# Kernel optimization log

Hardware: AMD Instinct MI355X
Metric: run time of the kernel (lower is better)

## Reference

```python
import jax, jax.numpy as jnp
import numpy as np

ROPE_BASE = 10000.0


def _rope_cos_sin(n, d, dtype):
    # standard llama-style rotary embedding over head dim d
    inv_freq = 1.0 / (ROPE_BASE ** (jnp.arange(0, d, 2, dtype=jnp.float32) / d))
    t = jnp.arange(n, dtype=jnp.float32)
    freqs = jnp.einsum('n,f->nf', t, inv_freq)          # [N, d/2]
    emb = jnp.concatenate([freqs, freqs], axis=-1)      # [N, d]
    return jnp.cos(emb).astype(dtype), jnp.sin(emb).astype(dtype)


def _rotate_half(x):
    x1, x2 = jnp.split(x, 2, axis=-1)
    return jnp.concatenate([-x2, x1], axis=-1)


def _apply_rope(x, cos, sin):
    # x: [B, H, N, D]; cos/sin: [N, D] broadcast over B, H
    return x * cos + _rotate_half(x) * sin


def setup_inputs() -> dict:
    key = jax.random.key(0)
    k1, k2, k3 = jax.random.split(key, 3)
    B, N, dim = 2, 2048, 1024
    heads, dim_head = 16, 64
    inner = heads * dim_head
    x = jax.random.normal(k1, (B, N, dim), dtype=jnp.float32)
    w_qkv = jax.random.normal(k2, (dim, 3 * inner), dtype=jnp.float32) * (dim ** -0.5)
    w_out = jax.random.normal(k3, (inner, dim), dtype=jnp.float32) * (inner ** -0.5)
    return {"x": x, "w_qkv": w_qkv, "w_out": w_out}


def reference(x, w_qkv, w_out):
    B, N, _ = x.shape
    heads, dim_head = 16, 64
    qkv = jnp.einsum('bnd,de->bne', x, w_qkv)
    q, k, v = jnp.split(qkv, 3, axis=-1)
    def to_heads(t):
        return t.reshape(B, N, heads, dim_head).transpose(0, 2, 1, 3)  # [B,H,N,D]
    q, k, v = to_heads(q), to_heads(k), to_heads(v)
    cos, sin = _rope_cos_sin(N, dim_head, x.dtype)
    q = _apply_rope(q, cos, sin)
    k = _apply_rope(k, cos, sin)
    scale = dim_head ** -0.5
    scores = jnp.einsum('bhqd,bhkd->bhqk', q, k) * scale   # [B,H,N,N], non-causal
    attn = jax.nn.softmax(scores, axis=-1)
    out = jnp.einsum('bhqk,bhkd->bhqd', attn, v)
    out = out.transpose(0, 2, 1, 3).reshape(B, N, heads * dim_head)
    return jnp.einsum('bne,ed->bnd', out, w_out)
```

## Files before the change

kernel.cpp:

```cpp
#include <hip/hip_runtime.h>

typedef __attribute__((ext_vector_type(8))) short bf16x8;
typedef __attribute__((ext_vector_type(4))) float f32x4;

#define MFMA(a, b, c) __builtin_amdgcn_mfma_f32_16x16x32_bf16(a, b, c, 0, 0, 0)

__device__ __forceinline__ unsigned short f2bf(float f) {
    unsigned u = __builtin_bit_cast(unsigned, f);
    u += 0x7fffu + ((u >> 16) & 1u);
    return (unsigned short)(u >> 16);
}

__device__ __forceinline__ void gload16(const unsigned short* g, unsigned short* l) {
    __builtin_amdgcn_global_load_lds(
        (const __attribute__((address_space(1))) void*)g,
        (__attribute__((address_space(3))) void*)l, 16, 0, 0);
}

__device__ __forceinline__ unsigned pack_bf16(float lo, float hi) {
    unsigned a = __builtin_bit_cast(unsigned, lo) + 0x8000u;
    unsigned b = __builtin_bit_cast(unsigned, hi) + 0x8000u;
    return __builtin_amdgcn_perm(b, a, 0x07060302);
}


__global__ __launch_bounds__(256) void cvt_bf16(const float* __restrict__ in,
                                                unsigned short* __restrict__ out, int n) {
    int i = (blockIdx.x * 256 + threadIdx.x) * 4;
    if (i < n) {
        float4 f = *(const float4*)(in + i);
        ushort4 u;
        u.x = f2bf(f.x); u.y = f2bf(f.y); u.z = f2bf(f.z); u.w = f2bf(f.w);
        *(ushort4*)(out + i) = u;
    }
}

__global__ __launch_bounds__(256) void transpose_cvt(const float* __restrict__ in,
                                                     unsigned short* __restrict__ out,
                                                     int R, int C) {
    __shared__ float tile[32][33];
    const int c0 = blockIdx.x * 32, r0 = blockIdx.y * 32;
    const int tr = threadIdx.x >> 3;
    const int j4 = (threadIdx.x & 7) * 4;
    float4 f = *(const float4*)(in + (size_t)(r0 + tr) * C + c0 + j4);
    tile[tr][j4 + 0] = f.x; tile[tr][j4 + 1] = f.y;
    tile[tr][j4 + 2] = f.z; tile[tr][j4 + 3] = f.w;
    __syncthreads();
    ushort4 u;
    u.x = f2bf(tile[j4 + 0][tr]); u.y = f2bf(tile[j4 + 1][tr]);
    u.z = f2bf(tile[j4 + 2][tr]); u.w = f2bf(tile[j4 + 3][tr]);
    *(ushort4*)(out + (size_t)(c0 + tr) * R + r0 + j4) = u;
}

__global__ __launch_bounds__(256) void rope_tab(float* __restrict__ cosT,
                                                float* __restrict__ sinT) {
    int i = blockIdx.x * 256 + threadIdx.x;
    int n = i >> 5, f = i & 31;
    float ang = (float)n * exp2f((float)f * -0.4152410118609203f);
    float s, c;
    sincosf(ang, &s, &c);
    cosT[i] = c; sinT[i] = s;
}


template <int EPI>
__global__ __launch_bounds__(256, 3) void gemm_bt(const unsigned short* __restrict__ A,
                                                  const unsigned short* __restrict__ Bt,
                                                  int K, int Ncols,
                                                  unsigned short* __restrict__ oq,
                                                  unsigned short* __restrict__ ok,
                                                  unsigned short* __restrict__ ovt,
                                                  float* __restrict__ of,
                                                  const float* __restrict__ cosT,
                                                  const float* __restrict__ sinT) {
    __shared__ unsigned short As[2][128 * 32];
    __shared__ unsigned short Bs[2][128 * 32];
    const int tid = threadIdx.x;
    const int w = tid >> 6, lane = tid & 63, quad = lane >> 4, cc = lane & 15;
    const int wm = w >> 1, wn = w & 1;
    const int m0 = blockIdx.y * 128, n0 = blockIdx.x * 128;

    size_t aoff[2], boff[2];
#pragma unroll
    for (int t = 0; t < 2; t++) {
        int S = w * 128 + t * 64 + lane;
        int row = S >> 2;
        int c = (S & 3) ^ ((row >> 1) & 3);
        aoff[t] = (size_t)(m0 + row) * K + c * 8;
        boff[t] = (size_t)(n0 + row) * K + c * 8;
    }

#pragma unroll
    for (int t = 0; t < 2; t++) {
        gload16(A + aoff[t], &As[0][(w * 2 + t) * 512]);
        gload16(Bt + boff[t], &Bs[0][(w * 2 + t) * 512]);
    }
    __syncthreads();

    f32x4 acc[4][4] = {};
    const int rpos = (quad ^ ((cc >> 1) & 3)) * 8;
    const int nkt = K >> 5;

    for (int kt = 0; kt < nkt; kt++) {
        const int pb = kt & 1;
        if (kt < nkt - 1) {
            const int ko = (kt + 1) * 32;
#pragma unroll
            for (int t = 0; t < 2; t++) {
                gload16(A + aoff[t] + ko, &As[pb ^ 1][(w * 2 + t) * 512]);
                gload16(Bt + boff[t] + ko, &Bs[pb ^ 1][(w * 2 + t) * 512]);
            }
        }
        bf16x8 af[4], bf[4];
#pragma unroll
        for (int i = 0; i < 4; i++)
            af[i] = *(const bf16x8*)&As[pb][(wm * 64 + i * 16 + cc) * 32 + rpos];
#pragma unroll
        for (int i = 0; i < 4; i++)
            bf[i] = *(const bf16x8*)&Bs[pb][(wn * 64 + i * 16 + cc) * 32 + rpos];
#pragma unroll
        for (int i = 0; i < 4; i++)
#pragma unroll
            for (int j = 0; j < 4; j++)
                acc[i][j] = MFMA(af[i], bf[j], acc[i][j]);
        __syncthreads();
    }

    if (EPI == 0) {
        const int e0 = n0 + wn * 64;
        const int which = e0 >> 10;
        const int h = (e0 >> 6) & 15;
        if (which < 2) {
            unsigned short* dst = (which == 0) ? oq : ok;
            const float postscale = (which == 0) ? 0.125f : 1.0f;
#pragma unroll
            for (int mf = 0; mf < 4; mf++) {
#pragma unroll
                for (int r = 0; r < 4; r++) {
                    int mg = m0 + wm * 64 + mf * 16 + quad * 4 + r;
                    int nseq = mg & 2047, b = mg >> 11;
                    float vals[4];
#pragma unroll
                    for (int nf = 0; nf < 4; nf++) vals[nf] = acc[mf][nf][r];
                    size_t rowbase = ((size_t)(b * 16 + h) * 2048 + nseq) * 64;
#pragma unroll
                    for (int nf = 0; nf < 4; nf++) {
                        int d = nf * 16 + cc;
                        int f = d & 31;
                        float cs = cosT[nseq * 32 + f];
                        float sn = sinT[nseq * 32 + f];
                        float partner = vals[nf ^ 2];
                        float outv = (vals[nf] * cs +
                                      ((nf < 2) ? -partner : partner) * sn) * postscale;
                        dst[rowbase + d] = f2bf(outv);
                    }
                }
            }
        } else {
#pragma unroll
            for (int mf = 0; mf < 4; mf++) {
                int mg0 = m0 + wm * 64 + mf * 16 + quad * 4;
                int b = mg0 >> 11, nseq = mg0 & 2047;
#pragma unroll
                for (int nf = 0; nf < 4; nf++) {
                    int d = nf * 16 + cc;
                    ushort4 pk;
                    pk.x = f2bf(acc[mf][nf][0]);
                    pk.y = f2bf(acc[mf][nf][1]);
                    pk.z = f2bf(acc[mf][nf][2]);
                    pk.w = f2bf(acc[mf][nf][3]);
                    *(ushort4*)(ovt + ((size_t)(b * 16 + h) * 64 + d) * 2048 + nseq) = pk;
                }
            }
        }
    } else {
#pragma unroll
        for (int mf = 0; mf < 4; mf++)
#pragma unroll
            for (int nf = 0; nf < 4; nf++)
#pragma unroll
                for (int r = 0; r < 4; r++) {
                    int mg = m0 + wm * 64 + mf * 16 + quad * 4 + r;
                    of[(size_t)mg * Ncols + n0 + wn * 64 + nf * 16 + cc] = acc[mf][nf][r];
                }
    }
}


__global__ __launch_bounds__(512, 4) void attn(const unsigned short* __restrict__ q,
                                               const unsigned short* __restrict__ k,
                                               const unsigned short* __restrict__ vt,
                                               unsigned short* __restrict__ o) {
    __shared__ unsigned short ks[2][64 * 64];
    __shared__ unsigned short vs[2][64 * 64];
    __shared__ unsigned short ps[128 * 72];
    __shared__ float rsb[128];
    const int tid = threadIdx.x;
    const int w = tid >> 6, lane = tid & 63, quad = lane >> 4, cc = lane & 15;
    const int bh = blockIdx.x & 31, qt = blockIdx.x >> 5;

    const unsigned short* qg = q + ((size_t)bh * 2048 + qt * 128 + w * 16) * 64;
    bf16x8 aq[2];
#pragma unroll
    for (int kc = 0; kc < 2; kc++)
        aq[kc] = *(const bf16x8*)(qg + cc * 64 + kc * 32 + quad * 8);

    const int S = w * 64 + lane;
    const int row = S >> 3;
    const int c = (S & 7) ^ (row & 7);
    const int koff = row * 64 + c * 8;
    const int voff = row * 2048 + c * 8;

    const unsigned short* kg0 = k + (size_t)bh * 2048 * 64;
    const unsigned short* vg0 = vt + (size_t)bh * 64 * 2048;

    gload16(kg0 + koff, &ks[0][w * 512]);
    gload16(vg0 + voff, &vs[0][w * 512]);
    __syncthreads();

    f32x4 oacc[4] = {};
    float rs = 0.f;

    for (int kt = 0; kt < 32; kt++) {
        const int pb = kt & 1;
        if (kt < 31) {
            const unsigned short* kb = kg0 + (kt + 1) * 4096;
            const unsigned short* vb = vg0 + (kt + 1) * 64;
            gload16(kb + koff, &ks[pb ^ 1][w * 512]);
            gload16(vb + voff, &vs[pb ^ 1][w * 512]);
        }

        f32x4 s2[4] = {};
        __builtin_amdgcn_s_setprio(1);
#pragma unroll
        for (int kc = 0; kc < 2; kc++) {
#pragma unroll
            for (int nf = 0; nf < 4; nf++) {
                bf16x8 bk = *(const bf16x8*)&ks[pb][(nf * 16 + cc) * 64 +
                                                    ((kc * 4 + quad) ^ (cc & 7)) * 8];
                s2[nf] = MFMA(bk, aq[kc], s2[nf]);
            }
        }
        __builtin_amdgcn_s_setprio(0);

#pragma unroll
        for (int nf = 0; nf < 4; nf++) {
            float p0 = __builtin_amdgcn_exp2f(
                __builtin_fmaf(s2[nf][0], 1.44269504f, -11.54156036f));
            float p1 = __builtin_amdgcn_exp2f(
                __builtin_fmaf(s2[nf][1], 1.44269504f, -11.54156036f));
            float p2 = __builtin_amdgcn_exp2f(
                __builtin_fmaf(s2[nf][2], 1.44269504f, -11.54156036f));
            float p3 = __builtin_amdgcn_exp2f(
                __builtin_fmaf(s2[nf][3], 1.44269504f, -11.54156036f));
            rs += (p0 + p1) + (p2 + p3);
            uint2 pk;
            pk.x = pack_bf16(p0, p1);
            pk.y = pack_bf16(p2, p3);
            *(uint2*)&ps[(w * 16 + cc) * 72 + nf * 16 + quad * 4] = pk;
        }

#pragma unroll
        for (int kc = 0; kc < 2; kc++) {
            bf16x8 ap = *(const bf16x8*)&ps[(w * 16 + cc) * 72 + kc * 32 + quad * 8];
            __builtin_amdgcn_s_setprio(1);
#pragma unroll
            for (int df = 0; df < 4; df++) {
                bf16x8 bv = *(const bf16x8*)&vs[pb][(df * 16 + cc) * 64 +
                                                    ((kc * 4 + quad) ^ (cc & 7)) * 8];
                oacc[df] = MFMA(ap, bv, oacc[df]);
            }
            __builtin_amdgcn_s_setprio(0);
        }

        __syncthreads();
    }

    rs += __shfl_xor(rs, 16, 64);
    rs += __shfl_xor(rs, 32, 64);
    if (quad == 0) rsb[w * 16 + cc] = rs;

    {
        f32x4 rv = *(const f32x4*)&rsb[w * 16 + quad * 4];
        f32x4 inv;
#pragma unroll
        for (int r = 0; r < 4; r++) inv[r] = 1.0f / rv[r];
#pragma unroll
        for (int r = 0; r < 4; r++)
#pragma unroll
            for (int df = 0; df < 4; df++)
                ps[(w * 16 + quad * 4 + r) * 72 + df * 16 + cc] =
                    f2bf(oacc[df][r] * inv[r]);
    }
    __syncthreads();
    {
        const int b = bh >> 4, h = bh & 15;
        int row2 = tid >> 2, seg = tid & 3;
        unsigned short* og =
            o + ((size_t)(b * 2048 + qt * 128 + row2)) * 1024 + h * 64 + seg * 16;
#pragma unroll
        for (int j = 0; j < 2; j++)
            *(uint4*)(og + j * 8) = *(const uint4*)&ps[row2 * 72 + seg * 16 + j * 8];
    }
}


extern "C" void kernel_launch(void* const* d_in, const int* in_sizes, int n_in,
                              void* d_out, int out_size, void* d_ws, size_t ws_size,
                              hipStream_t stream) {
    const float* x = (const float*)d_in[0];
    const float* w_qkv = (const float*)d_in[1];
    const float* w_out = (const float*)d_in[2];
    float* out = (float*)d_out;

    unsigned short* xb    = (unsigned short*)d_ws;
    unsigned short* wqkvT = xb + 4096 * 1024;
    unsigned short* woutT = wqkvT + 3072 * 1024;
    unsigned short* qb    = woutT + 1024 * 1024;
    unsigned short* kb    = qb + 2 * 16 * 2048 * 64;
    unsigned short* vtb   = kb + 2 * 16 * 2048 * 64;
    unsigned short* ob    = vtb + 2 * 16 * 2048 * 64;
    float* cosT = (float*)(ob + 4096 * 1024);
    float* sinT = cosT + 2048 * 32;

    rope_tab<<<256, 256, 0, stream>>>(cosT, sinT);
    cvt_bf16<<<4096, 256, 0, stream>>>(x, xb, 4096 * 1024);
    transpose_cvt<<<dim3(96, 32), 256, 0, stream>>>(w_qkv, wqkvT, 1024, 3072);
    transpose_cvt<<<dim3(32, 32), 256, 0, stream>>>(w_out, woutT, 1024, 1024);
    gemm_bt<0><<<dim3(24, 32), 256, 0, stream>>>(xb, wqkvT, 1024, 3072,
                                                 qb, kb, vtb, nullptr, cosT, sinT);
    attn<<<512, 512, 0, stream>>>(qb, kb, vtb, ob);
    gemm_bt<1><<<dim3(8, 32), 256, 0, stream>>>(ob, woutT, 1024, 1024,
                                                nullptr, nullptr, nullptr, out,
                                                nullptr, nullptr);
}
```

Measured before the change: 186.0 us.

## Software-pipeline QK and PV across iterations, keep P in registers via permlane

Restructures the attention loop so that the QK^T MFMAs for tile kt run alongside the PV MFMAs for tile kt-1. V loads are staggered one stage behind K. The softmax probabilities are no longer written to and reread from LDS; they are rearranged into the MFMA A-operand layout in registers with v_permlane32/16_swap. This aims to hide the exp latency and drop the LDS round trip, at the cost of higher register pressure and a correctness dependence on the permlane lane mapping.

```diff
diff --git a/kernel.cpp b/kernel.cpp
--- a/kernel.cpp
+++ b/kernel.cpp
@@ -215,34 +215,34 @@
     const unsigned short* vg0 = vt + (size_t)bh * 64 * 2048;
 
     gload16(kg0 + koff, &ks[0][w * 512]);
-    gload16(vg0 + voff, &vs[0][w * 512]);
     __syncthreads();
 
     f32x4 oacc[4] = {};
     float rs = 0.f;
-
-    for (int kt = 0; kt < 32; kt++) {
-        const int pb = kt & 1;
-        if (kt < 31) {
-            const unsigned short* kb = kg0 + (kt + 1) * 4096;
-            const unsigned short* vb = vg0 + (kt + 1) * 64;
-            gload16(kb + koff, &ks[pb ^ 1][w * 512]);
-            gload16(vb + voff, &vs[pb ^ 1][w * 512]);
-        }
-
-        f32x4 s2[4] = {};
-        __builtin_amdgcn_s_setprio(1);
-#pragma unroll
-        for (int kc = 0; kc < 2; kc++) {
+    bf16x8 apP[2];
+
+    auto qk = [&](const unsigned short* kbuf, f32x4 s2[4]) {
+#pragma unroll
+        for (int kc = 0; kc < 2; kc++)
 #pragma unroll
             for (int nf = 0; nf < 4; nf++) {
-                bf16x8 bk = *(const bf16x8*)&ks[pb][(nf * 16 + cc) * 64 +
-                                                    ((kc * 4 + quad) ^ (cc & 7)) * 8];
+                bf16x8 bk = *(const bf16x8*)&kbuf[(nf * 16 + cc) * 64 +
+                                                  ((kc * 4 + quad) ^ (cc & 7)) * 8];
                 s2[nf] = MFMA(bk, aq[kc], s2[nf]);
             }
-        }
-        __builtin_amdgcn_s_setprio(0);
-
+    };
+    auto pv = [&](const unsigned short* vbuf, const bf16x8 ap[2]) {
+#pragma unroll
+        for (int kc = 0; kc < 2; kc++)
+#pragma unroll
+            for (int df = 0; df < 4; df++) {
+                bf16x8 bv = *(const bf16x8*)&vbuf[(df * 16 + cc) * 64 +
+                                                  ((kc * 4 + quad) ^ (cc & 7)) * 8];
+                oacc[df] = MFMA(ap[kc], bv, oacc[df]);
+            }
+    };
+    auto softmax_pack = [&](const f32x4 s2[4], bf16x8 apC[2]) {
+        unsigned X[4][2];
 #pragma unroll
         for (int nf = 0; nf < 4; nf++) {
             float p0 = __builtin_amdgcn_exp2f(
@@ -254,27 +254,55 @@
             float p3 = __builtin_amdgcn_exp2f(
                 __builtin_fmaf(s2[nf][3], 1.44269504f, -11.54156036f));
             rs += (p0 + p1) + (p2 + p3);
-            uint2 pk;
-            pk.x = pack_bf16(p0, p1);
-            pk.y = pack_bf16(p2, p3);
-            *(uint2*)&ps[(w * 16 + cc) * 72 + nf * 16 + quad * 4] = pk;
+            X[nf][0] = pack_bf16(p0, p1);
+            X[nf][1] = pack_bf16(p2, p3);
         }
-
 #pragma unroll
         for (int kc = 0; kc < 2; kc++) {
-            bf16x8 ap = *(const bf16x8*)&ps[(w * 16 + cc) * 72 + kc * 32 + quad * 8];
-            __builtin_amdgcn_s_setprio(1);
-#pragma unroll
-            for (int df = 0; df < 4; df++) {
-                bf16x8 bv = *(const bf16x8*)&vs[pb][(df * 16 + cc) * 64 +
-                                                    ((kc * 4 + quad) ^ (cc & 7)) * 8];
-                oacc[df] = MFMA(ap, bv, oacc[df]);
-            }
-            __builtin_amdgcn_s_setprio(0);
+            unsigned a0 = X[kc * 2][0], b0 = X[kc * 2 + 1][0];
+            unsigned a1 = X[kc * 2][1], b1 = X[kc * 2 + 1][1];
+            asm("v_permlane32_swap_b32 %0, %1" : "+v"(a0), "+v"(b0));
+            asm("v_permlane16_swap_b32 %0, %1" : "+v"(a0), "+v"(b0));
+            asm("v_permlane32_swap_b32 %0, %1" : "+v"(a1), "+v"(b1));
+            asm("v_permlane16_swap_b32 %0, %1" : "+v"(a1), "+v"(b1));
+            uint4 dd;
+            dd.x = a0; dd.y = a1; dd.z = b0; dd.w = b1;
+            apC[kc] = __builtin_bit_cast(bf16x8, dd);
         }
-
+    };
+
+    gload16(kg0 + 4096 + koff, &ks[1][w * 512]);
+    gload16(vg0 + voff, &vs[0][w * 512]);
+    {
+        f32x4 s2[4] = {};
+        __builtin_amdgcn_s_setprio(1);
+        qk(ks[0], s2);
+        __builtin_amdgcn_s_setprio(0);
+        softmax_pack(s2, apP);
+    }
+    __syncthreads();
+
+    for (int kt = 1; kt < 32; kt++) {
+        if (kt < 31)
+            gload16(kg0 + (kt + 1) * 4096 + koff, &ks[(kt + 1) & 1][w * 512]);
+        gload16(vg0 + kt * 64 + voff, &vs[kt & 1][w * 512]);
+
+        f32x4 s2[4] = {};
+        __builtin_amdgcn_s_setprio(1);
+        qk(ks[kt & 1], s2);
+        pv(vs[(kt - 1) & 1], apP);
+        __builtin_amdgcn_s_setprio(0);
+
+        bf16x8 apC[2];
+        softmax_pack(s2, apC);
+        apP[0] = apC[0];
+        apP[1] = apC[1];
         __syncthreads();
     }
+
+    __builtin_amdgcn_s_setprio(1);
+    pv(vs[1], apP);
+    __builtin_amdgcn_s_setprio(0);
 
     rs += __shfl_xor(rs, 16, 64);
     rs += __shfl_xor(rs, 32, 64);
```

Result: no change. 188.1 us (+1.1%).

## Add dedicated 256x256 QKV GEMM with four-phase LDS pipeline and setprio

Applied to the files above, without the earlier changes.

Replaces the templated 128x128 QKV projection GEMM with a specialised 512-thread kernel. It uses 256x256 tiles, a 64-wide K step, an XOR-swizzled LDS layout and double buffering. Compute is split into four barrier-separated MFMA phases with raised wave priority. The aim is more operand reuse per LDS load and better overlap of global-to-LDS loads with MFMA. The trade-off is only 192 blocks, fewer than the CU count, plus higher register pressure. The output projection is split into its own non-templated kernel.

```diff
diff --git a/kernel.cpp b/kernel.cpp
--- a/kernel.cpp
+++ b/kernel.cpp
@@ -63,16 +63,151 @@
 }
 
 
-template <int EPI>
-__global__ __launch_bounds__(256, 3) void gemm_bt(const unsigned short* __restrict__ A,
-                                                  const unsigned short* __restrict__ Bt,
-                                                  int K, int Ncols,
-                                                  unsigned short* __restrict__ oq,
-                                                  unsigned short* __restrict__ ok,
-                                                  unsigned short* __restrict__ ovt,
-                                                  float* __restrict__ of,
-                                                  const float* __restrict__ cosT,
-                                                  const float* __restrict__ sinT) {
+#define PHASE(AB, BB, MH, NH, DOA, DOB)                                           \
+    do {                                                                          \
+        if (DOA) {                                                                \
+            _Pragma("unroll") for (int mf = 0; mf < 4; mf++)                      \
+                _Pragma("unroll") for (int kc = 0; kc < 2; kc++)                  \
+                    af[mf][kc] = *(const bf16x8*)&(AB)[                           \
+                        (wm * 128 + MH * 64 + mf * 16 + cc) * 64 +                \
+                        ((kc * 4 + quad) ^ (cc & 7)) * 8];                        \
+        }                                                                         \
+        if (DOB) {                                                                \
+            _Pragma("unroll") for (int nf = 0; nf < 2; nf++)                      \
+                _Pragma("unroll") for (int kc = 0; kc < 2; kc++)                  \
+                    bfr[nf][kc] = *(const bf16x8*)&(BB)[                          \
+                        (wn * 64 + NH * 32 + nf * 16 + cc) * 64 +                 \
+                        ((kc * 4 + quad) ^ (cc & 7)) * 8];                        \
+        }                                                                         \
+        __builtin_amdgcn_s_setprio(1);                                            \
+        _Pragma("unroll") for (int mf = 0; mf < 4; mf++)                          \
+            _Pragma("unroll") for (int nf = 0; nf < 2; nf++)                      \
+                _Pragma("unroll") for (int kc = 0; kc < 2; kc++)                  \
+                    acc[MH * 4 + mf][NH * 2 + nf] = MFMA(                         \
+                        af[mf][kc], bfr[nf][kc], acc[MH * 4 + mf][NH * 2 + nf]);  \
+        __builtin_amdgcn_s_setprio(0);                                            \
+    } while (0)
+
+__global__ __launch_bounds__(512, 2) void gemm_qkv(const unsigned short* __restrict__ A,
+                                                   const unsigned short* __restrict__ Bt,
+                                                   unsigned short* __restrict__ oq,
+                                                   unsigned short* __restrict__ ok,
+                                                   unsigned short* __restrict__ ovt,
+                                                   const float* __restrict__ cosT,
+                                                   const float* __restrict__ sinT) {
+    __shared__ unsigned short Ab[2][256 * 64];
+    __shared__ unsigned short Bb[2][256 * 64];
+    const int tid = threadIdx.x;
+    const int w = tid >> 6, lane = tid & 63, quad = lane >> 4, cc = lane & 15;
+    const int wm = w >> 2, wn = w & 3;
+    const int m0 = blockIdx.y * 256, n0 = blockIdx.x * 256;
+
+    int soff[4], lb[4];
+#pragma unroll
+    for (int j = 0; j < 4; j++) {
+        int S = j * 512 + w * 64 + lane;
+        int row = S >> 3;
+        int c = (S & 7) ^ (row & 7);
+        soff[j] = row * 1024 + c * 8;
+        lb[j] = (j * 512 + w * 64) * 8;
+    }
+    const unsigned short* Ag = A + (size_t)m0 * 1024;
+    const unsigned short* Bg = Bt + (size_t)n0 * 1024;
+
+    auto stage = [&](const unsigned short* g, unsigned short* l) {
+#pragma unroll
+        for (int j = 0; j < 4; j++) gload16(g + soff[j], l + lb[j]);
+    };
+
+    f32x4 acc[8][4] = {};
+    bf16x8 af[4][2], bfr[2][2];
+
+    stage(Ag, &Ab[0][0]);
+    stage(Bg, &Bb[0][0]);
+    asm volatile("s_waitcnt vmcnt(0)" ::: "memory");
+    __builtin_amdgcn_s_barrier();
+
+    for (int t = 0; t < 8; ++t) {
+        const int k0 = 2 * t;
+        stage(Ag + (k0 + 1) * 64, &Ab[1][0]);
+        stage(Bg + (k0 + 1) * 64, &Bb[1][0]);
+        PHASE(Ab[0], Bb[0], 0, 0, true, true);
+        __builtin_amdgcn_s_barrier();
+        PHASE(Ab[0], Bb[0], 0, 1, false, true);
+        __builtin_amdgcn_s_barrier();
+        PHASE(Ab[0], Bb[0], 1, 1, true, false);
+        __builtin_amdgcn_s_barrier();
+        PHASE(Ab[0], Bb[0], 1, 0, false, true);
+        asm volatile("s_waitcnt vmcnt(0)" ::: "memory");
+        __builtin_amdgcn_s_barrier();
+        if (t < 7) {
+            stage(Ag + (k0 + 2) * 64, &Ab[0][0]);
+            stage(Bg + (k0 + 2) * 64, &Bb[0][0]);
+        }
+        PHASE(Ab[1], Bb[1], 0, 0, true, true);
+        __builtin_amdgcn_s_barrier();
+        PHASE(Ab[1], Bb[1], 0, 1, false, true);
+        __builtin_amdgcn_s_barrier();
+        PHASE(Ab[1], Bb[1], 1, 1, true, false);
+        __builtin_amdgcn_s_barrier();
+        PHASE(Ab[1], Bb[1], 1, 0, false, true);
+        asm volatile("s_waitcnt vmcnt(0)" ::: "memory");
+        __builtin_amdgcn_s_barrier();
+    }
+
+    const int e0 = n0 + wn * 64;
+    const int which = e0 >> 10;
+    const int h = (e0 >> 6) & 15;
+    if (which < 2) {
+        unsigned short* dst = (which == 0) ? oq : ok;
+        const float postscale = (which == 0) ? 0.125f : 1.0f;
+#pragma unroll
+        for (int mf = 0; mf < 8; mf++) {
+#pragma unroll
+            for (int r = 0; r < 4; r++) {
+                int mg = m0 + wm * 128 + mf * 16 + quad * 4 + r;
+                int nseq = mg & 2047, b = mg >> 11;
+                float vals[4];
+#pragma unroll
+                for (int nf = 0; nf < 4; nf++) vals[nf] = acc[mf][nf][r];
+                size_t rowbase = ((size_t)(b * 16 + h) * 2048 + nseq) * 64;
+#pragma unroll
+                for (int nf = 0; nf < 4; nf++) {
+                    int d = nf * 16 + cc;
+                    int f = d & 31;
+                    float cs = cosT[nseq * 32 + f];
+                    float sn = sinT[nseq * 32 + f];
+                    float partner = vals[nf ^ 2];
+                    float outv = (vals[nf] * cs +
+                                  ((nf < 2) ? -partner : partner) * sn) * postscale;
+                    dst[rowbase + d] = f2bf(outv);
+                }
+            }
+        }
+    } else {
+#pragma unroll
+        for (int mf = 0; mf < 8; mf++) {
+            int mg0 = m0 + wm * 128 + mf * 16 + quad * 4;
+            int b = mg0 >> 11, nseq = mg0 & 2047;
+#pragma unroll
+            for (int nf = 0; nf < 4; nf++) {
+                int d = nf * 16 + cc;
+                ushort4 pk;
+                pk.x = f2bf(acc[mf][nf][0]);
+                pk.y = f2bf(acc[mf][nf][1]);
+                pk.z = f2bf(acc[mf][nf][2]);
+                pk.w = f2bf(acc[mf][nf][3]);
+                *(ushort4*)(ovt + ((size_t)(b * 16 + h) * 64 + d) * 2048 + nseq) = pk;
+            }
+        }
+    }
+}
+
+
+__global__ __launch_bounds__(256, 3) void gemm_out(const unsigned short* __restrict__ A,
+                                                   const unsigned short* __restrict__ Bt,
+                                                   int K, int Ncols,
+                                                   float* __restrict__ of) {
     __shared__ unsigned short As[2][128 * 32];
     __shared__ unsigned short Bs[2][128 * 32];
     const int tid = threadIdx.x;
@@ -111,79 +246,30 @@
                 gload16(Bt + boff[t] + ko, &Bs[pb ^ 1][(w * 2 + t) * 512]);
             }
         }
-        bf16x8 af[4], bf[4];
+        bf16x8 afv[4], bfv[4];
 #pragma unroll
         for (int i = 0; i < 4; i++)
-            af[i] = *(const bf16x8*)&As[pb][(wm * 64 + i * 16 + cc) * 32 + rpos];
+            afv[i] = *(const bf16x8*)&As[pb][(wm * 64 + i * 16 + cc) * 32 + rpos];
 #pragma unroll
         for (int i = 0; i < 4; i++)
-            bf[i] = *(const bf16x8*)&Bs[pb][(wn * 64 + i * 16 + cc) * 32 + rpos];
+            bfv[i] = *(const bf16x8*)&Bs[pb][(wn * 64 + i * 16 + cc) * 32 + rpos];
 #pragma unroll
         for (int i = 0; i < 4; i++)
 #pragma unroll
             for (int j = 0; j < 4; j++)
-                acc[i][j] = MFMA(af[i], bf[j], acc[i][j]);
+                acc[i][j] = MFMA(afv[i], bfv[j], acc[i][j]);
         __syncthreads();
     }
 
-    if (EPI == 0) {
-        const int e0 = n0 + wn * 64;
-        const int which = e0 >> 10;
-        const int h = (e0 >> 6) & 15;
-        if (which < 2) {
-            unsigned short* dst = (which == 0) ? oq : ok;
-            const float postscale = (which == 0) ? 0.125f : 1.0f;
-#pragma unroll
-            for (int mf = 0; mf < 4; mf++) {
-#pragma unroll
-                for (int r = 0; r < 4; r++) {
-                    int mg = m0 + wm * 64 + mf * 16 + quad * 4 + r;
-                    int nseq = mg & 2047, b = mg >> 11;
-                    float vals[4];
-#pragma unroll
-                    for (int nf = 0; nf < 4; nf++) vals[nf] = acc[mf][nf][r];
-                    size_t rowbase = ((size_t)(b * 16 + h) * 2048 + nseq) * 64;
-#pragma unroll
-                    for (int nf = 0; nf < 4; nf++) {
-                        int d = nf * 16 + cc;
-                        int f = d & 31;
-                        float cs = cosT[nseq * 32 + f];
-                        float sn = sinT[nseq * 32 + f];
-                        float partner = vals[nf ^ 2];
-                        float outv = (vals[nf] * cs +
-                                      ((nf < 2) ? -partner : partner) * sn) * postscale;
-                        dst[rowbase + d] = f2bf(outv);
-                    }
-                }
-            }
-        } else {
-#pragma unroll
-            for (int mf = 0; mf < 4; mf++) {
-                int mg0 = m0 + wm * 64 + mf * 16 + quad * 4;
-                int b = mg0 >> 11, nseq = mg0 & 2047;
-#pragma unroll
-                for (int nf = 0; nf < 4; nf++) {
-                    int d = nf * 16 + cc;
-                    ushort4 pk;
-                    pk.x = f2bf(acc[mf][nf][0]);
-                    pk.y = f2bf(acc[mf][nf][1]);
-                    pk.z = f2bf(acc[mf][nf][2]);
-                    pk.w = f2bf(acc[mf][nf][3]);
-                    *(ushort4*)(ovt + ((size_t)(b * 16 + h) * 64 + d) * 2048 + nseq) = pk;
-                }
-            }
-        }
-    } else {
-#pragma unroll
-        for (int mf = 0; mf < 4; mf++)
-#pragma unroll
-            for (int nf = 0; nf < 4; nf++)
-#pragma unroll
-                for (int r = 0; r < 4; r++) {
-                    int mg = m0 + wm * 64 + mf * 16 + quad * 4 + r;
-                    of[(size_t)mg * Ncols + n0 + wn * 64 + nf * 16 + cc] = acc[mf][nf][r];
-                }
-    }
+#pragma unroll
+    for (int mf = 0; mf < 4; mf++)
+#pragma unroll
+        for (int nf = 0; nf < 4; nf++)
+#pragma unroll
+            for (int r = 0; r < 4; r++) {
+                int mg = m0 + wm * 64 + mf * 16 + quad * 4 + r;
+                of[(size_t)mg * Ncols + n0 + wn * 64 + nf * 16 + cc] = acc[mf][nf][r];
+            }
 }
 
 
@@ -327,10 +413,7 @@
     cvt_bf16<<<4096, 256, 0, stream>>>(x, xb, 4096 * 1024);
     transpose_cvt<<<dim3(96, 32), 256, 0, stream>>>(w_qkv, wqkvT, 1024, 3072);
     transpose_cvt<<<dim3(32, 32), 256, 0, stream>>>(w_out, woutT, 1024, 1024);
-    gemm_bt<0><<<dim3(24, 32), 256, 0, stream>>>(xb, wqkvT, 1024, 3072,
-                                                 qb, kb, vtb, nullptr, cosT, sinT);
+    gemm_qkv<<<dim3(12, 16), 512, 0, stream>>>(xb, wqkvT, qb, kb, vtb, cosT, sinT);
     attn<<<512, 512, 0, stream>>>(qb, kb, vtb, ob);
-    gemm_bt<1><<<dim3(8, 32), 256, 0, stream>>>(ob, woutT, 1024, 1024,
-                                                nullptr, nullptr, nullptr, out,
-                                                nullptr, nullptr);
-}
+    gemm_out<<<dim3(8, 32), 256, 0, stream>>>(ob, woutT, 1024, 1024, out);
+}
```

New measurement: 191.0 us. +2.7%, slower.
